# Performance work log

Hardware: AMD Instinct MI355X
Metric: run time of the kernel (lower is better)

Reference implementation:

```python
import jax, jax.numpy as jnp
import numpy as np
from jax.scipy.linalg import expm

DIM = 64
TIMESTEPS = 1000
BATCH = 1024


def setup_inputs() -> dict:
    key = jax.random.key(0)
    k1, k2 = jax.random.split(key)
    inputs = jax.random.normal(k1, (BATCH, TIMESTEPS, DIM), dtype=jnp.float32)
    # Kernel: skew-symmetric (oscillatory) + small decay so expm(kernel*t) stays
    # bounded for t up to TIMESTEPS-1 (a random dense kernel would overflow).
    a = jax.random.normal(k2, (DIM, DIM), dtype=jnp.float32)
    kernel = 0.01 * (a - a.T) - 0.002 * jnp.eye(DIM, dtype=jnp.float32)
    return {"inputs": inputs, "kernel": kernel}


def reference(inputs, kernel):
    # matrix_exponentials[t] = expm(kernel * t), t = 0..T-1  -> [T, dim, dim]
    ts = jnp.arange(TIMESTEPS, dtype=kernel.dtype)
    mexp = jax.vmap(expm)(kernel[None, :, :] * ts[:, None, None])
    # trajs = einsum('tij,bj->bti'): propagate initial state inputs[:, 0, :]
    x0 = inputs[:, 0, :]  # [B, dim]
    return jnp.einsum('tij,bj->bti', mexp, x0)  # [B, T, dim]
```

## Files before the change

### kernel.cpp

```cpp
#include <hip/hip_runtime.h>

#define NMAT 1000
#define SA_PAD 68

#define SEEDF_OFF 2048000
#define X0B_OFF   8355840

typedef short short8 __attribute__((ext_vector_type(8)));
typedef float floatx4 __attribute__((ext_vector_type(4)));
typedef unsigned short ushortx4 __attribute__((ext_vector_type(4)));

__device__ __forceinline__ unsigned short f2bf(float f) {
    unsigned int u = __float_as_uint(f);
    u += 0x7fffu + ((u >> 16) & 1u);
    return (unsigned short)(u >> 16);
}

__device__ __forceinline__ void mm_core(const float* __restrict__ sA,
                                        const float* __restrict__ sB,
                                        int r0, int c0, float acc[4][4])
{
#pragma unroll
    for (int k = 0; k < 64; k += 4) {
        float4 b0 = *(const float4*)&sB[(k + 0) * SA_PAD + c0];
        float4 b1 = *(const float4*)&sB[(k + 1) * SA_PAD + c0];
        float4 b2 = *(const float4*)&sB[(k + 2) * SA_PAD + c0];
        float4 b3 = *(const float4*)&sB[(k + 3) * SA_PAD + c0];
#pragma unroll
        for (int u = 0; u < 4; ++u) {
            float4 a = *(const float4*)&sA[(r0 + u) * SA_PAD + k];
            acc[u][0] += a.x * b0.x + a.y * b1.x + a.z * b2.x + a.w * b3.x;
            acc[u][1] += a.x * b0.y + a.y * b1.y + a.z * b2.y + a.w * b3.y;
            acc[u][2] += a.x * b0.z + a.y * b1.z + a.z * b2.z + a.w * b3.z;
            acc[u][3] += a.x * b0.w + a.y * b1.w + a.z * b2.w + a.w * b3.w;
        }
    }
}

__device__ __forceinline__ void stageLDS(float* __restrict__ s, const float* __restrict__ g, int tid)
{
#pragma unroll
    for (int q = 0; q < 4; ++q) {
        int i4 = tid + 256 * q;
        int r = i4 >> 4, c4 = (i4 & 15) * 4;
        *(float4*)&s[r * SA_PAD + c4] = *(const float4*)&g[i4 * 4];
    }
}

__global__ __launch_bounds__(256) void k_build(const float* __restrict__ K,
                                               const float* __restrict__ in,
                                               float* __restrict__ ws)
{
    const int tid = threadIdx.x;
    unsigned short* tab16 = (unsigned short*)ws;
    unsigned short* x0b = (unsigned short*)((char*)ws + X0B_OFF);

    if (blockIdx.x != 0) {
        const int rb = (blockIdx.x - 1) * 64;
#pragma unroll
        for (int q = 0; q < 4; ++q) {
            int i4 = tid + 256 * q;
            int b = rb + (i4 >> 4), c4 = (i4 & 15) * 4;
            float4 v = *(const float4*)&in[(size_t)b * 64000 + c4];
            ushortx4 h = { f2bf(v.x), f2bf(v.y), f2bf(v.z), f2bf(v.w) };
            *(ushortx4*)&x0b[(size_t)b * 64 + c4] = h;
        }
        return;
    }

    __shared__ __align__(16) float smem[6 * 64 * SA_PAD];

#pragma unroll
    for (int q = 0; q < 4; ++q) {
        int i4 = tid + 256 * q;
        int r = i4 >> 4, c4 = (i4 & 15) * 4;
        *(float4*)&smem[r * SA_PAD + c4] = *(const float4*)&K[i4 * 4];
        ushortx4 id = {0, 0, 0, 0};
        if (r >= c4 && r < c4 + 4) ((unsigned short*)&id)[r - c4] = 0x3F80;
        *(ushortx4*)&tab16[r * 64 + c4] = id;
    }

    const float c1_ = 1.f, c2_ = 0.5f, c3_ = 1.f / 6.f, c4_ = 1.f / 24.f, c5_ = 1.f / 120.f,
                c6_ = 1.f / 720.f, c7_ = 1.f / 5040.f, c8_ = 1.f / 40320.f, c9_ = 1.f / 362880.f,
                c10_ = 1.f / 3628800.f, c11_ = 1.f / 39916800.f, c12_ = 1.f / 479001600.f;

    const signed char SD[14]  = {1, 2, 3, 5, 4, 5, 0, 1, 2, 3, 4, 5, 0, 1};
    const signed char SAi[14] = {0, 1, 1, 4, 5, 4, 5, 0, 1, 2, 3, 4, 5, 0};
    const signed char SBi[14] = {0, 0, 1, 3, 3, 4, 5, 0, 1, 2, 3, 4, 5, 0};
    const signed char SE[14]  = {-1, -1, -1, 0, 1, -1, -1, -1, -1, -1, -1, -1, -1, -1};
    const short       STt[14] = {-1, -1, -1, -1, 1, 2, 4, 8, 16, 32, 64, 128, 256, 512};

    const int r0 = (tid >> 4) * 4, c0 = (tid & 15) * 4;

#pragma unroll 1
    for (int st = 0; st < 14; ++st) {
        if (st == 3) {
            __syncthreads();
#pragma unroll
            for (int s = 0; s < 16; ++s) {
                int idx = tid + 256 * s;
                int r = idx >> 6, c = idx & 63;
                smem[4 * (64 * SA_PAD) + r * SA_PAD + c] =
                      c12_ * smem[3 * (64 * SA_PAD) + r * SA_PAD + c] + (r == c ? c8_ : 0.f)
                    + c9_  * smem[0 * (64 * SA_PAD) + r * SA_PAD + c]
                    + c10_ * smem[1 * (64 * SA_PAD) + r * SA_PAD + c]
                    + c11_ * smem[2 * (64 * SA_PAD) + r * SA_PAD + c];
            }
        }
        __syncthreads();
        const float* A = smem + (int)SAi[st] * (64 * SA_PAD);
        const float* B = smem + (int)SBi[st] * (64 * SA_PAD);
        float acc[4][4] = {};
        mm_core(A, B, r0, c0, acc);

        float cI = 0.f, cK = 0.f, cT2 = 0.f, cT3 = 0.f;
        const int epi = SE[st];
        if (epi == 0) { cI = c4_; cK = c5_; cT2 = c6_; cT3 = c7_; }
        if (epi == 1) { cI = 1.f; cK = c1_; cT2 = c2_; cT3 = c3_; }

        float* D = smem + (int)SD[st] * (64 * SA_PAD);
        float* sf = (STt[st] >= 0) ? (ws + SEEDF_OFF + (size_t)(st - 4) * 4096) : nullptr;
        unsigned short* tb = (STt[st] >= 0) ? (tab16 + (size_t)STt[st] * 4096) : nullptr;
#pragma unroll
        for (int u = 0; u < 4; ++u) {
            int r = r0 + u;
            float o[4];
#pragma unroll
            for (int v = 0; v < 4; ++v) {
                int c = c0 + v;
                float val = acc[u][v];
                if (epi >= 0) {
                    val += (r == c ? cI : 0.f)
                         + cK  * smem[0 * (64 * SA_PAD) + r * SA_PAD + c]
                         + cT2 * smem[1 * (64 * SA_PAD) + r * SA_PAD + c]
                         + cT3 * smem[2 * (64 * SA_PAD) + r * SA_PAD + c];
                }
                o[v] = val;
            }
            float4 vv = {o[0], o[1], o[2], o[3]};
            *(float4*)&D[r * SA_PAD + c0] = vv;
            if (sf) {
                *(float4*)&sf[r * 64 + c0] = vv;
                ushortx4 h = { f2bf(o[0]), f2bf(o[1]), f2bf(o[2]), f2bf(o[3]) };
                *(ushortx4*)&tb[r * 64 + c0] = h;
            }
        }
    }
}

__global__ __launch_bounds__(256) void k_pows(float* __restrict__ ws)
{
    __shared__ __align__(16) float s0[64 * SA_PAD], s1[64 * SA_PAD], s2[64 * SA_PAD];
    const int t = blockIdx.x;
    if (__popc(t) < 2) return;
    const float* seedF = ws + SEEDF_OFF;
    unsigned short* tab16 = (unsigned short*)ws;
    const int tid = threadIdx.x;
    const int r0 = (tid >> 4) * 4, c0 = (tid & 15) * 4;

    float* P = s0;
    float* Bs = s1;
    float* Cs = s2;

    int hb = 31 - __clz(t);
    stageLDS(P, seedF + (size_t)hb * 4096, tid);
    int rem = t & ~(1 << hb);

    float4 rg[4];
    {
        int b = 31 - __clz(rem);
        rem &= ~(1 << b);
        const float* g = seedF + (size_t)b * 4096;
#pragma unroll
        for (int q = 0; q < 4; ++q) rg[q] = *(const float4*)&g[(tid + 256 * q) * 4];
    }

    while (true) {
        __syncthreads();
#pragma unroll
        for (int q = 0; q < 4; ++q) {
            int i4 = tid + 256 * q;
            int rr = i4 >> 4, c4 = (i4 & 15) * 4;
            *(float4*)&Bs[rr * SA_PAD + c4] = rg[q];
        }
        int nb = -1;
        if (rem) {
            nb = 31 - __clz(rem);
            rem &= ~(1 << nb);
            const float* g = seedF + (size_t)nb * 4096;
#pragma unroll
            for (int q = 0; q < 4; ++q) rg[q] = *(const float4*)&g[(tid + 256 * q) * 4];
        }
        __syncthreads();
        float acc[4][4] = {};
        mm_core(P, Bs, r0, c0, acc);

        if (nb < 0) {
            unsigned short* C = tab16 + (size_t)t * 4096;
#pragma unroll
            for (int u = 0; u < 4; ++u) {
                ushortx4 h = { f2bf(acc[u][0]), f2bf(acc[u][1]),
                               f2bf(acc[u][2]), f2bf(acc[u][3]) };
                *(ushortx4*)&C[(r0 + u) * 64 + c0] = h;
            }
            return;
        }
#pragma unroll
        for (int u = 0; u < 4; ++u) {
            float4 vv = {acc[u][0], acc[u][1], acc[u][2], acc[u][3]};
            *(float4*)&Cs[(r0 + u) * SA_PAD + c0] = vv;
        }
        float* tmp = P; P = Cs; Cs = tmp;
    }
}

__global__ __launch_bounds__(256) void k_out(const float* __restrict__ ws,
                                             float* __restrict__ out)
{
    const unsigned short* tab16 = (const unsigned short*)ws;
    const unsigned short* x0b = (const unsigned short*)((const char*)ws + X0B_OFF);

    const int bx = blockIdx.x;
    const int tg = bx >> 4;
    const int bt = bx & 15;
    const int tid = threadIdx.x;
    const int lane = tid & 63;
    const int w = tid >> 6;
    const int m = lane & 15;
    const int kg = lane >> 4;

    const int b = bt * 64 + w * 16 + m;
    const int t0 = tg * 8;

    short8 xb0 = *(const short8*)&x0b[(size_t)b * 64 + kg * 8];
    short8 xb1 = *(const short8*)&x0b[(size_t)b * 64 + 32 + kg * 8];

    float* outb = out + (size_t)b * 64000 + (size_t)t0 * 64;

#pragma unroll 2
    for (int tt = 0; tt < 8; ++tt) {
        const unsigned short* Mt = tab16 + (size_t)(t0 + tt) * 4096;
        short8 ma[4][2];
#pragma unroll
        for (int n = 0; n < 4; ++n) {
            ma[n][0] = *(const short8*)&Mt[(n * 16 + m) * 64 + kg * 8];
            ma[n][1] = *(const short8*)&Mt[(n * 16 + m) * 64 + 32 + kg * 8];
        }
#pragma unroll
        for (int n = 0; n < 4; ++n) {
            floatx4 acc = {0.f, 0.f, 0.f, 0.f};
            acc = __builtin_amdgcn_mfma_f32_16x16x32_bf16(ma[n][0], xb0, acc, 0, 0, 0);
            acc = __builtin_amdgcn_mfma_f32_16x16x32_bf16(ma[n][1], xb1, acc, 0, 0, 0);
            *(floatx4*)&outb[(size_t)tt * 64 + n * 16 + kg * 4] = acc;
        }
    }
}

extern "C" void kernel_launch(void* const* d_in, const int* in_sizes, int n_in,
                              void* d_out, int out_size, void* d_ws, size_t ws_size,
                              hipStream_t stream)
{
    const float* inp = (const float*)d_in[0];
    const float* K   = (const float*)d_in[1];
    float* out = (float*)d_out;
    float* ws  = (float*)d_ws;

    hipLaunchKernelGGL(k_build, dim3(17), dim3(256), 0, stream, K, inp, ws);
    hipLaunchKernelGGL(k_pows, dim3(NMAT), dim3(256), 0, stream, ws);
    hipLaunchKernelGGL(k_out, dim3(2000), dim3(256), 0, stream, ws, out);
}
```

Measured before the change: 627.6 us.

## Fuse matrix-power chain with output MFMA to drop the bf16 table

```diff
diff --git a/kernel.cpp b/kernel.cpp
--- a/kernel.cpp
+++ b/kernel.cpp
@@ -14,6 +14,15 @@
     unsigned int u = __float_as_uint(f);
     u += 0x7fffu + ((u >> 16) & 1u);
     return (unsigned short)(u >> 16);
+}
+
+__device__ __forceinline__ short8 pack_bf8(float4 a, float4 b) {
+    short8 r;
+    r[0] = (short)f2bf(a.x); r[1] = (short)f2bf(a.y);
+    r[2] = (short)f2bf(a.z); r[3] = (short)f2bf(a.w);
+    r[4] = (short)f2bf(b.x); r[5] = (short)f2bf(b.y);
+    r[6] = (short)f2bf(b.z); r[7] = (short)f2bf(b.w);
+    return r;
 }
 
 __device__ __forceinline__ void mm_core(const float* __restrict__ sA,
@@ -52,7 +61,6 @@
                                                float* __restrict__ ws)
 {
     const int tid = threadIdx.x;
-    unsigned short* tab16 = (unsigned short*)ws;
     unsigned short* x0b = (unsigned short*)((char*)ws + X0B_OFF);
 
     if (blockIdx.x != 0) {
@@ -75,9 +83,6 @@
         int i4 = tid + 256 * q;
         int r = i4 >> 4, c4 = (i4 & 15) * 4;
         *(float4*)&smem[r * SA_PAD + c4] = *(const float4*)&K[i4 * 4];
-        ushortx4 id = {0, 0, 0, 0};
-        if (r >= c4 && r < c4 + 4) ((unsigned short*)&id)[r - c4] = 0x3F80;
-        *(ushortx4*)&tab16[r * 64 + c4] = id;
     }
 
     const float c1_ = 1.f, c2_ = 0.5f, c3_ = 1.f / 6.f, c4_ = 1.f / 24.f, c5_ = 1.f / 120.f,
@@ -88,7 +93,7 @@
     const signed char SAi[14] = {0, 1, 1, 4, 5, 4, 5, 0, 1, 2, 3, 4, 5, 0};
     const signed char SBi[14] = {0, 0, 1, 3, 3, 4, 5, 0, 1, 2, 3, 4, 5, 0};
     const signed char SE[14]  = {-1, -1, -1, 0, 1, -1, -1, -1, -1, -1, -1, -1, -1, -1};
-    const short       STt[14] = {-1, -1, -1, -1, 1, 2, 4, 8, 16, 32, 64, 128, 256, 512};
+    const signed char SSd[14] = {-1, -1, -1, -1, 0, 1, 2, 3, 4, 5, 6, 7, 8, 9};
 
     const int r0 = (tid >> 4) * 4, c0 = (tid & 15) * 4;
 
@@ -119,8 +124,7 @@
         if (epi == 1) { cI = 1.f; cK = c1_; cT2 = c2_; cT3 = c3_; }
 
         float* D = smem + (int)SD[st] * (64 * SA_PAD);
-        float* sf = (STt[st] >= 0) ? (ws + SEEDF_OFF + (size_t)(st - 4) * 4096) : nullptr;
-        unsigned short* tb = (STt[st] >= 0) ? (tab16 + (size_t)STt[st] * 4096) : nullptr;
+        float* sf = (SSd[st] >= 0) ? (ws + SEEDF_OFF + (size_t)SSd[st] * 4096) : nullptr;
 #pragma unroll
         for (int u = 0; u < 4; ++u) {
             int r = r0 + u;
@@ -139,119 +143,113 @@
             }
             float4 vv = {o[0], o[1], o[2], o[3]};
             *(float4*)&D[r * SA_PAD + c0] = vv;
-            if (sf) {
-                *(float4*)&sf[r * 64 + c0] = vv;
-                ushortx4 h = { f2bf(o[0]), f2bf(o[1]), f2bf(o[2]), f2bf(o[3]) };
-                *(ushortx4*)&tb[r * 64 + c0] = h;
-            }
-        }
-    }
-}
-
-__global__ __launch_bounds__(256) void k_pows(float* __restrict__ ws)
-{
-    __shared__ __align__(16) float s0[64 * SA_PAD], s1[64 * SA_PAD], s2[64 * SA_PAD];
+            if (sf) *(float4*)&sf[r * 64 + c0] = vv;
+        }
+    }
+}
+
+__global__ __launch_bounds__(256) void k_fused(const float* __restrict__ ws,
+                                               float* __restrict__ out)
+{
+    __shared__ __align__(16) float P[64 * SA_PAD];
+    __shared__ __align__(16) float Bs[64 * SA_PAD];
+
     const int t = blockIdx.x;
-    if (__popc(t) < 2) return;
+    const int tid = threadIdx.x;
+    const unsigned short* x0b = (const unsigned short*)((const char*)ws + X0B_OFF);
+
+    if (t == 0) {
+#pragma unroll 1
+        for (int q = 0; q < 64; ++q) {
+            int i4 = tid + 256 * q;
+            int b = i4 >> 4, c4 = (i4 & 15) * 4;
+            ushortx4 h = *(const ushortx4*)&x0b[(size_t)b * 64 + c4];
+            float4 v;
+            v.x = __uint_as_float((unsigned)(unsigned short)h[0] << 16);
+            v.y = __uint_as_float((unsigned)(unsigned short)h[1] << 16);
+            v.z = __uint_as_float((unsigned)(unsigned short)h[2] << 16);
+            v.w = __uint_as_float((unsigned)(unsigned short)h[3] << 16);
+            *(float4*)&out[(size_t)b * 64000 + c4] = v;
+        }
+        return;
+    }
+
     const float* seedF = ws + SEEDF_OFF;
-    unsigned short* tab16 = (unsigned short*)ws;
-    const int tid = threadIdx.x;
     const int r0 = (tid >> 4) * 4, c0 = (tid & 15) * 4;
-
-    float* P = s0;
-    float* Bs = s1;
-    float* Cs = s2;
 
     int hb = 31 - __clz(t);
     stageLDS(P, seedF + (size_t)hb * 4096, tid);
     int rem = t & ~(1 << hb);
 
-    float4 rg[4];
-    {
-        int b = 31 - __clz(rem);
-        rem &= ~(1 << b);
-        const float* g = seedF + (size_t)b * 4096;
-#pragma unroll
-        for (int q = 0; q < 4; ++q) rg[q] = *(const float4*)&g[(tid + 256 * q) * 4];
-    }
-
-    while (true) {
-        __syncthreads();
-#pragma unroll
-        for (int q = 0; q < 4; ++q) {
-            int i4 = tid + 256 * q;
-            int rr = i4 >> 4, c4 = (i4 & 15) * 4;
-            *(float4*)&Bs[rr * SA_PAD + c4] = rg[q];
-        }
-        int nb = -1;
-        if (rem) {
-            nb = 31 - __clz(rem);
-            rem &= ~(1 << nb);
-            const float* g = seedF + (size_t)nb * 4096;
+    if (rem) {
+        float4 rg[4];
+        {
+            int b = 31 - __clz(rem); rem &= ~(1 << b);
+            const float* g = seedF + (size_t)b * 4096;
 #pragma unroll
             for (int q = 0; q < 4; ++q) rg[q] = *(const float4*)&g[(tid + 256 * q) * 4];
         }
-        __syncthreads();
-        float acc[4][4] = {};
-        mm_core(P, Bs, r0, c0, acc);
-
-        if (nb < 0) {
-            unsigned short* C = tab16 + (size_t)t * 4096;
+        while (true) {
+            __syncthreads();
+#pragma unroll
+            for (int q = 0; q < 4; ++q) {
+                int i4 = tid + 256 * q;
+                int rr = i4 >> 4, c4 = (i4 & 15) * 4;
+                *(float4*)&Bs[rr * SA_PAD + c4] = rg[q];
+            }
+            int nb = -1;
+            if (rem) {
+                nb = 31 - __clz(rem); rem &= ~(1 << nb);
+                const float* g = seedF + (size_t)nb * 4096;
+#pragma unroll
+                for (int q = 0; q < 4; ++q) rg[q] = *(const float4*)&g[(tid + 256 * q) * 4];
+            }
+            __syncthreads();
+            float acc[4][4] = {};
+            mm_core(P, Bs, r0, c0, acc);
+            __syncthreads();
 #pragma unroll
             for (int u = 0; u < 4; ++u) {
-                ushortx4 h = { f2bf(acc[u][0]), f2bf(acc[u][1]),
-                               f2bf(acc[u][2]), f2bf(acc[u][3]) };
-                *(ushortx4*)&C[(r0 + u) * 64 + c0] = h;
-            }
-            return;
-        }
-#pragma unroll
-        for (int u = 0; u < 4; ++u) {
-            float4 vv = {acc[u][0], acc[u][1], acc[u][2], acc[u][3]};
-            *(float4*)&Cs[(r0 + u) * SA_PAD + c0] = vv;
-        }
-        float* tmp = P; P = Cs; Cs = tmp;
-    }
-}
-
-__global__ __launch_bounds__(256) void k_out(const float* __restrict__ ws,
-                                             float* __restrict__ out)
-{
-    const unsigned short* tab16 = (const unsigned short*)ws;
-    const unsigned short* x0b = (const unsigned short*)((const char*)ws + X0B_OFF);
-
-    const int bx = blockIdx.x;
-    const int tg = bx >> 4;
-    const int bt = bx & 15;
-    const int tid = threadIdx.x;
+                float4 vv = {acc[u][0], acc[u][1], acc[u][2], acc[u][3]};
+                *(float4*)&P[(r0 + u) * SA_PAD + c0] = vv;
+            }
+            if (nb < 0) break;
+        }
+    }
+    __syncthreads();
+
     const int lane = tid & 63;
     const int w = tid >> 6;
     const int m = lane & 15;
     const int kg = lane >> 4;
 
-    const int b = bt * 64 + w * 16 + m;
-    const int t0 = tg * 8;
-
-    short8 xb0 = *(const short8*)&x0b[(size_t)b * 64 + kg * 8];
-    short8 xb1 = *(const short8*)&x0b[(size_t)b * 64 + 32 + kg * 8];
-
-    float* outb = out + (size_t)b * 64000 + (size_t)t0 * 64;
-
-#pragma unroll 2
-    for (int tt = 0; tt < 8; ++tt) {
-        const unsigned short* Mt = tab16 + (size_t)(t0 + tt) * 4096;
-        short8 ma[4][2];
-#pragma unroll
-        for (int n = 0; n < 4; ++n) {
-            ma[n][0] = *(const short8*)&Mt[(n * 16 + m) * 64 + kg * 8];
-            ma[n][1] = *(const short8*)&Mt[(n * 16 + m) * 64 + 32 + kg * 8];
-        }
-#pragma unroll
-        for (int n = 0; n < 4; ++n) {
-            floatx4 acc = {0.f, 0.f, 0.f, 0.f};
-            acc = __builtin_amdgcn_mfma_f32_16x16x32_bf16(ma[n][0], xb0, acc, 0, 0, 0);
-            acc = __builtin_amdgcn_mfma_f32_16x16x32_bf16(ma[n][1], xb1, acc, 0, 0, 0);
-            *(floatx4*)&outb[(size_t)tt * 64 + n * 16 + kg * 4] = acc;
+    short8 ma[4][2];
+#pragma unroll
+    for (int n = 0; n < 4; ++n) {
+        const float* row = &P[(n * 16 + m) * SA_PAD];
+        float4 f0 = *(const float4*)&row[kg * 8];
+        float4 f1 = *(const float4*)&row[kg * 8 + 4];
+        ma[n][0] = pack_bf8(f0, f1);
+        float4 g0 = *(const float4*)&row[32 + kg * 8];
+        float4 g1 = *(const float4*)&row[32 + kg * 8 + 4];
+        ma[n][1] = pack_bf8(g0, g1);
+    }
+
+#pragma unroll 1
+    for (int p = 0; p < 8; ++p) {
+#pragma unroll
+        for (int mt = 0; mt < 2; ++mt) {
+            const int b = p * 128 + w * 32 + mt * 16 + m;
+            short8 xb0 = *(const short8*)&x0b[(size_t)b * 64 + kg * 8];
+            short8 xb1 = *(const short8*)&x0b[(size_t)b * 64 + 32 + kg * 8];
+            float* outb = out + (size_t)b * 64000 + (size_t)t * 64;
+#pragma unroll
+            for (int n = 0; n < 4; ++n) {
+                floatx4 acc = {0.f, 0.f, 0.f, 0.f};
+                acc = __builtin_amdgcn_mfma_f32_16x16x32_bf16(ma[n][0], xb0, acc, 0, 0, 0);
+                acc = __builtin_amdgcn_mfma_f32_16x16x32_bf16(ma[n][1], xb1, acc, 0, 0, 0);
+                *(floatx4*)&outb[n * 16 + kg * 4] = acc;
+            }
         }
     }
 }
@@ -266,6 +264,5 @@
     float* ws  = (float*)d_ws;
 
     hipLaunchKernelGGL(k_build, dim3(17), dim3(256), 0, stream, K, inp, ws);
-    hipLaunchKernelGGL(k_pows, dim3(NMAT), dim3(256), 0, stream, ws);
-    hipLaunchKernelGGL(k_out, dim3(2000), dim3(256), 0, stream, ws, out);
-}
+    hipLaunchKernelGGL(k_fused, dim3(NMAT), dim3(256), 0, stream, ws, out);
+}
```

Result: faster. 614.8 us (-2.0%).
